# Performance work log

Measured on AMD Instinct MI355X. Metric: run time of the kernel, lower is better.

## Reference

```python
import jax, jax.numpy as jnp
import numpy as np

D = 1024

def setup_inputs() -> dict:
    key = jax.random.key(0)
    ks = jax.random.split(key, 9)
    B, S = 4, 2048
    s = 1.0 / np.sqrt(D)
    return {
        "query": jax.random.normal(ks[0], (B, S, D), jnp.float32),
        "key": jax.random.normal(ks[1], (B, S, D), jnp.float32),
        "value": jax.random.normal(ks[2], (B, S, D), jnp.float32),
        "Wq": jax.random.normal(ks[3], (D, D), jnp.float32) * s,
        "bq": jax.random.normal(ks[4], (D,), jnp.float32) * 0.01,
        "Wk": jax.random.normal(ks[5], (D, D), jnp.float32) * s,
        "bk": jax.random.normal(ks[6], (D,), jnp.float32) * 0.01,
        "Wv": jax.random.normal(ks[7], (D, D), jnp.float32) * s,
        "bv": jax.random.normal(ks[8], (D,), jnp.float32) * 0.01,
    }

def reference(query, key, value, Wq, bq, Wk, bk, Wv, bv):
    scale = 1.0 / (query.shape[-1] ** 0.5)
    q = jnp.einsum('bsd,ed->bse', query, Wq) + bq  # nn.Linear: x @ W.T + b
    k = jnp.einsum('bsd,ed->bse', key, Wk) + bk
    v = jnp.einsum('bsd,ed->bse', value, Wv) + bv
    scores = jnp.einsum('bqd,bkd->bqk', q, k) * scale  # [B, Sq, Skv]
    w = jax.nn.softmax(scores, axis=-1)
    return jnp.einsum('bqk,bkd->bqd', w, v)
```

## Files before the change

### kernel.cpp

```cpp
#include <hip/hip_runtime.h>

typedef __bf16 bf16x8 __attribute__((ext_vector_type(8)));
typedef float f32x4 __attribute__((ext_vector_type(4)));
typedef unsigned short u16x8 __attribute__((ext_vector_type(8)));

__device__ inline unsigned short f2bf(float f) {
  union { float f; unsigned u; } a; a.f = f;
  return (unsigned short)((a.u + 0x7fffu + ((a.u >> 16) & 1u)) >> 16);
}
__device__ inline float bf2f(unsigned short h) {
  union { unsigned u; float f; } a; a.u = ((unsigned)h) << 16;
  return a.f;
}

__global__ __launch_bounds__(256) void cvtW(const float* __restrict__ Wq,
                                            const float* __restrict__ Wk,
                                            const float* __restrict__ Wv,
                                            unsigned short* __restrict__ Wb) {
  int i = blockIdx.x * 256 + threadIdx.x;
  int idx = i >> 18;
  int off = i & 262143;
  const float* s = (idx == 0) ? Wq : ((idx == 1) ? Wk : Wv);
  float4 v = ((const float4*)s)[off];
  ushort4 o;
  o.x = f2bf(v.x); o.y = f2bf(v.y); o.z = f2bf(v.z); o.w = f2bf(v.w);
  ((ushort4*)(Wb + idx * 1048576))[off] = o;
}

#define G2L(gp, lp) __builtin_amdgcn_global_load_lds( \
    (const __attribute__((address_space(1))) void*)(gp), \
    (__attribute__((address_space(3))) void*)(lp), 16, 0, 0)

#define MFMA_(d, a, b) d = __builtin_amdgcn_mfma_f32_16x16x32_bf16(a, b, d, 0, 0, 0)
#define SB0() __builtin_amdgcn_sched_barrier(0)
#define LGKM(n) do { asm volatile("s_waitcnt lgkmcnt(" #n ")" ::: "memory"); SB0(); } while (0)
#define VMC(n) do { asm volatile("s_waitcnt vmcnt(" #n ")" ::: "memory"); SB0(); } while (0)

struct PJ {
  const float* A0; const float* A1; const float* A2;
  const unsigned short* B;
  unsigned short* outQ; unsigned short* outK; unsigned short* outV;
  const float* biasQ; const float* biasK; const float* biasV;
};

__global__ __launch_bounds__(256) void gemmP(PJ p) {
  extern __shared__ char smem[];
  char* smA = smem;
  char* smB = smem + 32768;
  const int tid = threadIdx.x, lane = tid & 63, wid = tid >> 6;
  const int wm = wid >> 1, wn = wid & 1;

  int orig = blockIdx.x + 8 * (blockIdx.y + 64 * blockIdx.z);
  int wg = (orig & 7) * 192 + (orig >> 3);
  int bx = wg & 7; int t2 = wg >> 3; int by = t2 & 63; int z = t2 >> 6;
  const int m0 = by << 7, n0 = bx << 7;

  const float* Az = (z == 0) ? p.A0 : ((z == 1) ? p.A1 : p.A2);

  const char* srcA0 = (const char*)Az + ((long long)m0 + (tid >> 4)) * 4096
                    + ((tid & 15) << 4);
  const int trow = tid >> 3;
  const int cs = (((tid & 7) ^ (trow & 7)) << 4);
  const char* srcB = (const char*)(p.B + (long long)z * 1048576
                                   + (long long)(n0 + trow) * 1024) + cs;

  const int aRowB = (((wm << 6) + (lane & 15)) << 7);
  const int bRowB = (((wn << 6) + (lane & 15)) << 7);
  const int csw = (lane & 7) << 4;
  const int ck0 = (((lane >> 4) << 4)) ^ csw;
  const int ck1 = ((((lane >> 4) << 4)) | 64) ^ csw;

  f32x4 acc[4][4];
#pragma unroll
  for (int i = 0; i < 4; ++i)
#pragma unroll
    for (int j = 0; j < 4; ++j) acc[i][j] = (f32x4){0.f, 0.f, 0.f, 0.f};

  float4 aregA[8], aregB[8];
  bf16x8 aLo[2][2], aHi[2][2], bLo[2][2], bHi[2][2];

  auto ldA = [&](int t, float4 (&ar)[8]) {
    const char* s = srcA0 + (long long)t * 256;
#pragma unroll
    for (int c = 0; c < 8; ++c)
      ar[c] = *(const float4*)(s + (long long)c * 65536);
  };
  auto wrA = [&](int t, float4 (&ar)[8]) {
    char* dA = smA + ((t & 1) << 14);
    const int g = (tid & 15) >> 1;
    const int hb = (tid & 1) << 3;
#pragma unroll
    for (int c = 0; c < 8; ++c) {
      const int rc = (c << 4) + (tid >> 4);
      float4 v = ar[c];
      union { __bf16 b[4]; ushort4 u; } o;
      o.b[0] = (__bf16)v.x; o.b[1] = (__bf16)v.y;
      o.b[2] = (__bf16)v.z; o.b[3] = (__bf16)v.w;
      *(ushort4*)(dA + (rc << 7) + ((g ^ (rc & 7)) << 4) + hb) = o.u;
    }
  };
  auto stageB = [&](int t, int b) {
    char* dB = smB + (b << 14) + (tid << 4);
    const char* sB = srcB + (long long)t * 128;
#pragma unroll
    for (int c = 0; c < 4; ++c)
      G2L(sB + (long long)c * 65536, dB + (c << 12));
  };
  auto readAh = [&](int b, int half, bf16x8 (&dst)[2][2]) {
    const char* ra = smA + (b << 14) + aRowB + (half << 12);
#pragma unroll
    for (int mi = 0; mi < 2; ++mi) {
      dst[mi][0] = *(const bf16x8*)(ra + (mi << 11) + ck0);
      dst[mi][1] = *(const bf16x8*)(ra + (mi << 11) + ck1);
    }
  };
  auto readBh = [&](int b, int half, bf16x8 (&dst)[2][2]) {
    const char* rb = smB + (b << 14) + bRowB + (half << 12);
#pragma unroll
    for (int ni = 0; ni < 2; ++ni) {
      dst[ni][0] = *(const bf16x8*)(rb + (ni << 11) + ck0);
      dst[ni][1] = *(const bf16x8*)(rb + (ni << 11) + ck1);
    }
  };
  auto quad = [&](int qa, int qb, bf16x8 (&A)[2][2], bf16x8 (&B)[2][2]) {
    __builtin_amdgcn_s_setprio(1);
#pragma unroll
    for (int mi = 0; mi < 2; ++mi)
#pragma unroll
      for (int ni = 0; ni < 2; ++ni) {
        MFMA_(acc[qa * 2 + mi][qb * 2 + ni], A[mi][0], B[ni][0]);
        MFMA_(acc[qa * 2 + mi][qb * 2 + ni], A[mi][1], B[ni][1]);
      }
    __builtin_amdgcn_s_setprio(0);
  };

  const int NT = 16;
  int b0 = 0, b1 = 1, b2 = 2;

  ldA(0, aregA); stageB(0, 0);
  ldA(1, aregB); stageB(1, 1);
  VMC(12);
  wrA(0, aregA);
  LGKM(0);
  __builtin_amdgcn_s_barrier();
  readAh(0, 0, aLo); readBh(0, 0, bLo);
  SB0();

  auto body = [&](int t, float4 (&arW)[8], float4 (&arL)[8]) {
    const bool pf1 = (t + 1) < NT, pf2 = (t + 2) < NT;
    if (pf2) { ldA(t + 2, arL); stageB(t + 2, b2); }
    readAh(t & 1, 1, aHi);
    SB0();
    LGKM(4);
    quad(0, 0, aLo, bLo);
    readBh(b0, 1, bHi);
    SB0();
    LGKM(4);
    quad(1, 0, aHi, bLo);
    LGKM(0);
    quad(0, 1, aLo, bHi);
    quad(1, 1, aHi, bHi);
    if (pf2) { VMC(12); }
    else     { VMC(0);  }
    if (pf1) wrA(t + 1, arW);
    LGKM(0);
    __builtin_amdgcn_s_barrier();
    if (pf1) { readAh((t + 1) & 1, 0, aLo); readBh(b1, 0, bLo); }
    SB0();
    int tmp = b0; b0 = b1; b1 = b2; b2 = tmp;
  };
  for (int t = 0; t < NT; t += 2) { body(t, aregB, aregA); body(t + 1, aregA, aregB); }

  const int c0 = lane & 15, r0 = (lane >> 4) << 2;
  if (z < 2) {
    unsigned short* O = (z == 0) ? p.outQ : p.outK;
    const float* bias = (z == 0) ? p.biasQ : p.biasK;
#pragma unroll
    for (int mi = 0; mi < 4; ++mi) {
      const int grow = m0 + (wm << 6) + (mi << 4) + r0;
#pragma unroll
      for (int ni = 0; ni < 4; ++ni) {
        const int gcol = n0 + (wn << 6) + (ni << 4) + c0;
        const float bb = bias[gcol];
#pragma unroll
        for (int rr = 0; rr < 4; ++rr)
          O[(long long)(grow + rr) * 1024 + gcol] = f2bf(acc[mi][ni][rr] + bb);
      }
    }
  } else {
#pragma unroll
    for (int mi = 0; mi < 4; ++mi) {
      const int grow = m0 + (wm << 6) + (mi << 4) + r0;
      const int bb = grow >> 11, s = grow & 2047;
#pragma unroll
      for (int ni = 0; ni < 4; ++ni) {
        const int d = n0 + (wn << 6) + (ni << 4) + c0;
        const float ba = p.biasV[d];
        ushort4 pk;
        pk.x = f2bf(acc[mi][ni][0] + ba);
        pk.y = f2bf(acc[mi][ni][1] + ba);
        pk.z = f2bf(acc[mi][ni][2] + ba);
        pk.w = f2bf(acc[mi][ni][3] + ba);
        *(ushort4*)(p.outV + ((long long)bb << 21) + (long long)d * 2048 + s) = pk;
      }
    }
  }
}

#define EPI_SCALE 1
#define EPI_OUT 2

struct GP {
  const unsigned short* A;
  const unsigned short* B;
  unsigned short* C;
  long long batchA, batchB, batchC;
  int lda, ldb, ldc, K;
  float scale;
};

template<int BM, int BN, int WMW, int WNW, int EPI>
__global__ __launch_bounds__(512, 2) void gemm2(GP p) {
  constexpr int NWN = BN / WNW;
  constexpr int AMF = WMW / 16, BNF = WNW / 16;
  constexpr int AH = AMF / 2, BH = BNF / 2;
  constexpr int AF_N = AH * 2;
  constexpr int NBA = BM / 64, NBB = BN / 64;
  static_assert((BM / WMW) * NWN == 8, "8 waves");
  static_assert(BNF == 4, "lgkm immediates assume BNF==4");

  extern __shared__ char smem[];
  char* smA = smem;
  char* smB = smem + 2 * BM * 128;

  const int tid = threadIdx.x;
  const int lane = tid & 63;
  const int wid = tid >> 6;
  const int wm = wid / NWN, wn = wid % NWN;

  const int gx = gridDim.x, gy = gridDim.y;
  const int nwg = gx * gy * (int)gridDim.z;
  int orig = blockIdx.x + gx * (blockIdx.y + gy * blockIdx.z);
  int qq = nwg >> 3, rr_ = nwg & 7;
  int xcd = orig & 7, sl = orig >> 3;
  int wg = (xcd < rr_ ? xcd * (qq + 1) : rr_ * (qq + 1) + (xcd - rr_) * qq) + sl;
  int bx = wg % gx;
  int t2 = wg / gx;
  int by = t2 % gy;
  int z  = t2 / gy;

  const int m0 = by * BM, n0 = bx * BN;

  const long long lda2 = (long long)p.lda * 2;
  const long long ldb2 = (long long)p.ldb * 2;
  const char* Abase = (const char*)(p.A + (long long)z * p.batchA) + (long long)m0 * lda2;
  const char* Bbase = (const char*)(p.B + (long long)z * p.batchB) + (long long)n0 * ldb2;

  const int trow = tid >> 3;
  const int cs = (((tid & 7) ^ (trow & 7)) << 4);
  const char* srcA = Abase + (long long)trow * lda2 + cs;
  const char* srcB = Bbase + (long long)trow * ldb2 + cs;

  const int NT = p.K >> 6;

  const int aRowB = ((wm * WMW + (lane & 15)) << 7);
  const int bRowB = ((wn * WNW + (lane & 15)) << 7);
  const int csw = (lane & 7) << 4;
  const int ck0 = (((lane >> 4) << 4)) ^ csw;
  const int ck1 = ((((lane >> 4) << 4)) | 64) ^ csw;

  f32x4 acc[AMF][BNF];
#pragma unroll
  for (int i = 0; i < AMF; ++i)
#pragma unroll
    for (int j = 0; j < BNF; ++j) acc[i][j] = (f32x4){0.f, 0.f, 0.f, 0.f};

  bf16x8 aLo[AH][2], aHi[AH][2], bLo[BH][2], bHi[BH][2];

  auto stage = [&](int t) {
    char* dA = smA + (t & 1) * (BM * 128) + (tid << 4);
    char* dB = smB + (t & 1) * (BN * 128) + (tid << 4);
    const char* sA = srcA + (long long)t * 128;
    const char* sB = srcB + (long long)t * 128;
#pragma unroll
    for (int c = 0; c < NBA; ++c) G2L(sA + (long long)c * (lda2 << 6), dA + c * 8192);
#pragma unroll
    for (int c = 0; c < NBB; ++c) G2L(sB + (long long)c * (ldb2 << 6), dB + c * 8192);
  };
  auto readAh = [&](int t, int half, bf16x8 (&dst)[AH][2]) {
    const char* ra = smA + (t & 1) * (BM * 128) + aRowB + half * (AH * 2048);
#pragma unroll
    for (int mi = 0; mi < AH; ++mi) {
      dst[mi][0] = *(const bf16x8*)(ra + mi * 2048 + ck0);
      dst[mi][1] = *(const bf16x8*)(ra + mi * 2048 + ck1);
    }
  };
  auto readBh = [&](int t, int half, bf16x8 (&dst)[BH][2]) {
    const char* rb = smB + (t & 1) * (BN * 128) + bRowB + half * (BH * 2048);
#pragma unroll
    for (int ni = 0; ni < BH; ++ni) {
      dst[ni][0] = *(const bf16x8*)(rb + ni * 2048 + ck0);
      dst[ni][1] = *(const bf16x8*)(rb + ni * 2048 + ck1);
    }
  };
  auto quad = [&](int qa, int qb, bf16x8 (&A)[AH][2], bf16x8 (&B)[BH][2]) {
    __builtin_amdgcn_s_setprio(1);
#pragma unroll
    for (int mi = 0; mi < AH; ++mi)
#pragma unroll
      for (int ni = 0; ni < BH; ++ni) {
        MFMA_(acc[qa * AH + mi][qb * BH + ni], A[mi][0], B[ni][0]);
        MFMA_(acc[qa * AH + mi][qb * BH + ni], A[mi][1], B[ni][1]);
      }
    __builtin_amdgcn_s_setprio(0);
  };

  stage(0); stage(1);
  if constexpr (NBA + NBB == 8) VMC(8); else VMC(6);
  __builtin_amdgcn_s_barrier();
  readAh(0, 0, aLo); readBh(0, 0, bLo);
  SB0();

  for (int t = 0; t < NT; ++t) {
    readAh(t, 1, aHi);
    SB0();
    if constexpr (AF_N == 8) LGKM(8); else LGKM(4);
    quad(0, 0, aLo, bLo);
    readBh(t, 1, bHi);
    SB0();
    LGKM(4);
    quad(1, 0, aHi, bLo);
    LGKM(0);
    quad(0, 1, aLo, bHi);
    quad(1, 1, aHi, bHi);
    VMC(0);
    __builtin_amdgcn_s_barrier();
    if (t + 2 < NT) stage(t + 2);
    if (t + 1 < NT) { readAh(t + 1, 0, aLo); readBh(t + 1, 0, bLo); }
    SB0();
  }

  const int c0 = lane & 15;
  const int r0 = (lane >> 4) << 2;
  if constexpr (EPI == EPI_SCALE) {
    unsigned short* Cz = p.C + (long long)z * p.batchC;
#pragma unroll
    for (int mi = 0; mi < AMF; ++mi) {
      const int grow = m0 + wm * WMW + (mi << 4) + r0;
#pragma unroll
      for (int ni = 0; ni < BNF; ++ni) {
        const int gcol = n0 + wn * WNW + (ni << 4) + c0;
#pragma unroll
        for (int rr = 0; rr < 4; ++rr)
          Cz[(long long)(grow + rr) * p.ldc + gcol] = f2bf(acc[mi][ni][rr] * p.scale);
      }
    }
  } else {
    float* Cz = (float*)p.C + (long long)z * p.batchC;
#pragma unroll
    for (int mi = 0; mi < AMF; ++mi) {
      const int grow = m0 + wm * WMW + (mi << 4) + r0;
#pragma unroll
      for (int ni = 0; ni < BNF; ++ni) {
        const int gcol = n0 + wn * WNW + (ni << 4) + c0;
#pragma unroll
        for (int rr = 0; rr < 4; ++rr)
          Cz[(long long)(grow + rr) * p.ldc + gcol] = acc[mi][ni][rr] * p.scale;
      }
    }
  }
}

__global__ __launch_bounds__(512) void gemmPV(GP p) {
  constexpr int ABUF = 256 * 128, BBUF = 128 * 128;
  extern __shared__ char smem[];
  char* smA = smem;
  char* smB = smem + 3 * ABUF;

  const int tid = threadIdx.x;
  const int lane = tid & 63;
  const int wid = tid >> 6;
  const int wm = wid >> 1, wn = wid & 1;

  const int gx = gridDim.x, gy = gridDim.y;
  const int nwg = gx * gy * (int)gridDim.z;
  int orig = blockIdx.x + gx * (blockIdx.y + gy * blockIdx.z);
  int qq = nwg >> 3, rr_ = nwg & 7;
  int xcd = orig & 7, sl = orig >> 3;
  int wg = (xcd < rr_ ? xcd * (qq + 1) : rr_ * (qq + 1) + (xcd - rr_) * qq) + sl;
  int bx = wg % gx;
  int t2 = wg / gx;
  int by = t2 % gy;
  int z  = t2 / gy;

  const int m0 = by * 256, n0 = bx * 128;

  const long long lda2 = (long long)p.lda * 2;
  const long long ldb2 = (long long)p.ldb * 2;
  const char* Abase = (const char*)(p.A + (long long)z * p.batchA) + (long long)m0 * lda2;
  const char* Bbase = (const char*)(p.B + (long long)z * p.batchB) + (long long)n0 * ldb2;

  const int trow = tid >> 3;
  const int cs = (((tid & 7) ^ (trow & 7)) << 4);
  const char* srcA = Abase + (long long)trow * lda2 + cs;
  const char* srcB = Bbase + (long long)trow * ldb2 + cs;

  const int NT = p.K >> 6;

  const int aRowB = ((wm * 64 + (lane & 15)) << 7);
  const int bRowB = ((wn * 64 + (lane & 15)) << 7);
  const int csw = (lane & 7) << 4;
  const int ck0 = (((lane >> 4) << 4)) ^ csw;
  const int ck1 = ((((lane >> 4) << 4)) | 64) ^ csw;

  f32x4 acc[4][4];
#pragma unroll
  for (int i = 0; i < 4; ++i)
#pragma unroll
    for (int j = 0; j < 4; ++j) acc[i][j] = (f32x4){0.f, 0.f, 0.f, 0.f};

  bf16x8 aLo[2][2], aHi[2][2], bLo[2][2], bHi[2][2];

  auto stage = [&](int t, int b) {
    char* dA = smA + b * ABUF + (tid << 4);
    char* dB = smB + b * BBUF + (tid << 4);
    const char* sA = srcA + (long long)t * 128;
    const char* sB = srcB + (long long)t * 128;
#pragma unroll
    for (int c = 0; c < 4; ++c) G2L(sA + (long long)c * (lda2 << 6), dA + c * 8192);
#pragma unroll
    for (int c = 0; c < 2; ++c) G2L(sB + (long long)c * (ldb2 << 6), dB + c * 8192);
  };
  auto readAh = [&](int b, int half, bf16x8 (&dst)[2][2]) {
    const char* ra = smA + b * ABUF + aRowB + half * 4096;
#pragma unroll
    for (int mi = 0; mi < 2; ++mi) {
      dst[mi][0] = *(const bf16x8*)(ra + mi * 2048 + ck0);
      dst[mi][1] = *(const bf16x8*)(ra + mi * 2048 + ck1);
    }
  };
  auto readBh = [&](int b, int half, bf16x8 (&dst)[2][2]) {
    const char* rb = smB + b * BBUF + bRowB + half * 4096;
#pragma unroll
    for (int ni = 0; ni < 2; ++ni) {
      dst[ni][0] = *(const bf16x8*)(rb + ni * 2048 + ck0);
      dst[ni][1] = *(const bf16x8*)(rb + ni * 2048 + ck1);
    }
  };
  auto quad = [&](int qa, int qb, bf16x8 (&A)[2][2], bf16x8 (&B)[2][2]) {
    __builtin_amdgcn_s_setprio(1);
#pragma unroll
    for (int mi = 0; mi < 2; ++mi)
#pragma unroll
      for (int ni = 0; ni < 2; ++ni) {
        MFMA_(acc[qa * 2 + mi][qb * 2 + ni], A[mi][0], B[ni][0]);
        MFMA_(acc[qa * 2 + mi][qb * 2 + ni], A[mi][1], B[ni][1]);
      }
    __builtin_amdgcn_s_setprio(0);
  };

  int b0 = 0, b1 = 1, b2 = 2;

  stage(0, 0); stage(1, 1);
  VMC(6);
  __builtin_amdgcn_s_barrier();
  readAh(0, 0, aLo); readBh(0, 0, bLo);
  SB0();

  for (int t = 0; t < NT; ++t) {
    if (t + 2 < NT) stage(t + 2, b2);
    readAh(b0, 1, aHi);
    SB0();
    LGKM(4);
    quad(0, 0, aLo, bLo);
    readBh(b0, 1, bHi);
    SB0();
    LGKM(4);
    quad(1, 0, aHi, bLo);
    LGKM(0);
    quad(0, 1, aLo, bHi);
    quad(1, 1, aHi, bHi);
    if (t + 2 < NT) { VMC(6); }
    else            { VMC(0); }
    __builtin_amdgcn_s_barrier();
    if (t + 1 < NT) { readAh(b1, 0, aLo); readBh(b1, 0, bLo); }
    SB0();
    int tmp = b0; b0 = b1; b1 = b2; b2 = tmp;
  }

  const int c0 = lane & 15;
  const int r0 = (lane >> 4) << 2;
  float* Cz = (float*)p.C + (long long)z * p.batchC;
#pragma unroll
  for (int mi = 0; mi < 4; ++mi) {
    const int grow = m0 + wm * 64 + (mi << 4) + r0;
#pragma unroll
    for (int ni = 0; ni < 4; ++ni) {
      const int gcol = n0 + wn * 64 + (ni << 4) + c0;
#pragma unroll
      for (int rr = 0; rr < 4; ++rr)
        Cz[(long long)(grow + rr) * p.ldc + gcol] = acc[mi][ni][rr] * p.scale;
    }
  }
}

__global__ __launch_bounds__(256) void softmax_rows(unsigned short* __restrict__ S) {
  const size_t row = blockIdx.x;
  unsigned short* pp = S + row * 2048;
  const int t = threadIdx.x, lane = t & 63, wave = t >> 6;
  u16x8 h = ((const u16x8*)pp)[t];
  float x[8];
#pragma unroll
  for (int j = 0; j < 8; ++j) x[j] = bf2f(h[j]);
  float m = x[0];
#pragma unroll
  for (int j = 1; j < 8; ++j) m = fmaxf(m, x[j]);
#pragma unroll
  for (int off = 32; off >= 1; off >>= 1) m = fmaxf(m, __shfl_xor(m, off, 64));
  __shared__ float rmax[4], rsum[4];
  if (lane == 0) rmax[wave] = m;
  __syncthreads();
  m = fmaxf(fmaxf(rmax[0], rmax[1]), fmaxf(rmax[2], rmax[3]));
  float e[8], sum = 0.f;
#pragma unroll
  for (int j = 0; j < 8; ++j) { e[j] = __expf(x[j] - m); sum += e[j]; }
#pragma unroll
  for (int off = 32; off >= 1; off >>= 1) sum += __shfl_xor(sum, off, 64);
  if (lane == 0) rsum[wave] = sum;
  __syncthreads();
  sum = rsum[0] + rsum[1] + rsum[2] + rsum[3];
  const float inv = 1.f / sum;
  u16x8 o;
#pragma unroll
  for (int j = 0; j < 8; ++j) o[j] = f2bf(e[j] * inv);
  ((u16x8*)pp)[t] = o;
}

extern "C" void kernel_launch(void* const* d_in, const int* in_sizes, int n_in,
                              void* d_out, int out_size, void* d_ws, size_t ws_size,
                              hipStream_t stream) {
  const float* q  = (const float*)d_in[0];
  const float* k  = (const float*)d_in[1];
  const float* v  = (const float*)d_in[2];
  const float* Wq = (const float*)d_in[3];
  const float* bq = (const float*)d_in[4];
  const float* Wk = (const float*)d_in[5];
  const float* bk = (const float*)d_in[6];
  const float* Wv = (const float*)d_in[7];
  const float* bv = (const float*)d_in[8];

  unsigned short* S  = (unsigned short*)d_ws;
  unsigned short* Wb = S + 16777216;
  unsigned short* qb = Wb + 3145728;
  unsigned short* kb = qb + 8388608;
  unsigned short* vT = kb + 8388608;

  (void)hipFuncSetAttribute((const void*)gemmP,
      hipFuncAttributeMaxDynamicSharedMemorySize, 81920);
  (void)hipFuncSetAttribute((const void*)gemm2<256,256,128,64,EPI_SCALE>,
      hipFuncAttributeMaxDynamicSharedMemorySize, 131072);
  (void)hipFuncSetAttribute((const void*)gemmPV,
      hipFuncAttributeMaxDynamicSharedMemorySize, 147456);

  cvtW<<<3072, 256, 0, stream>>>(Wq, Wk, Wv, Wb);

  PJ pj{};
  pj.A0 = q; pj.A1 = k; pj.A2 = v;
  pj.B = Wb;
  pj.outQ = qb; pj.outK = kb; pj.outV = vT;
  pj.biasQ = bq; pj.biasK = bk; pj.biasV = bv;
  gemmP<<<dim3(8, 64, 3), 256, 81920, stream>>>(pj);

  GP gs{};
  gs.A = qb; gs.batchA = 2097152; gs.lda = 1024;
  gs.B = kb; gs.batchB = 2097152; gs.ldb = 1024;
  gs.C = S;  gs.batchC = 4194304; gs.ldc = 2048;
  gs.K = 1024; gs.scale = 0.03125f;
  gemm2<256,256,128,64,EPI_SCALE><<<dim3(8, 8, 4), 512, 131072, stream>>>(gs);

  softmax_rows<<<8192, 256, 0, stream>>>(S);

  GP gv{};
  gv.A = S;  gv.batchA = 4194304; gv.lda = 2048;
  gv.B = vT; gv.batchB = 2097152; gv.ldb = 2048;
  gv.C = (unsigned short*)d_out; gv.batchC = 2097152; gv.ldc = 1024;
  gv.K = 2048; gv.scale = 1.f;
  gemmPV<<<dim3(8, 8, 4), 512, 147456, stream>>>(gv);
}
```

Baseline: 167.3 us.

## Halve projection GEMM K-tile to 32 with paired-row swizzled LDS layout

The QKV projection GEMM now uses a K step of 32 instead of 64 per iteration (32 iterations instead of 16). Two 64-byte rows are packed into each 128-byte LDS row with a new XOR swizzle, and the A/B staging and fragment reads are rewritten to match. Dynamic shared memory drops from 80KB to 40KB and per-thread prefetch registers are halved, which should allow more resident workgroups per CU. The cost is twice as many barriers and loop iterations, plus less work per synchronization.

```diff
diff --git a/kernel.cpp b/kernel.cpp
--- a/kernel.cpp
+++ b/kernel.cpp
@@ -46,7 +46,7 @@
 __global__ __launch_bounds__(256) void gemmP(PJ p) {
   extern __shared__ char smem[];
   char* smA = smem;
-  char* smB = smem + 32768;
+  char* smB = smem + 16384;
   const int tid = threadIdx.x, lane = tid & 63, wid = tid >> 6;
   const int wm = wid >> 1, wn = wid & 1;
 
@@ -57,18 +57,20 @@
 
   const float* Az = (z == 0) ? p.A0 : ((z == 1) ? p.A1 : p.A2);
 
-  const char* srcA0 = (const char*)Az + ((long long)m0 + (tid >> 4)) * 4096
-                    + ((tid & 15) << 4);
-  const int trow = tid >> 3;
-  const int cs = (((tid & 7) ^ (trow & 7)) << 4);
+  const char* srcA0 = (const char*)Az + ((long long)m0 + (tid >> 3)) * 4096
+                    + ((tid & 7) << 4);
+  const int L0 = tid >> 3;
+  const int sgB = (tid & 7) ^ (L0 & 7);
   const char* srcB = (const char*)(p.B + (long long)z * 1048576
-                                   + (long long)(n0 + trow) * 1024) + cs;
-
-  const int aRowB = (((wm << 6) + (lane & 15)) << 7);
-  const int bRowB = (((wn << 6) + (lane & 15)) << 7);
-  const int csw = (lane & 7) << 4;
-  const int ck0 = (((lane >> 4) << 4)) ^ csw;
-  const int ck1 = ((((lane >> 4) << 4)) | 64) ^ csw;
+                     + (long long)(n0 + 2 * L0 + (sgB >> 2)) * 1024)
+                   + ((sgB & 3) << 4);
+
+  const int kqW = (tid & 7) >> 1;
+  const int hW = (tid & 1) << 3;
+
+  const int kh = lane >> 4;
+  const int Ra0 = (wm << 6) + (lane & 15);
+  const int Rb0 = (wn << 6) + (lane & 15);
 
   f32x4 acc[4][4];
 #pragma unroll
@@ -76,96 +78,96 @@
 #pragma unroll
     for (int j = 0; j < 4; ++j) acc[i][j] = (f32x4){0.f, 0.f, 0.f, 0.f};
 
-  float4 aregA[8], aregB[8];
-  bf16x8 aLo[2][2], aHi[2][2], bLo[2][2], bHi[2][2];
-
-  auto ldA = [&](int t, float4 (&ar)[8]) {
-    const char* s = srcA0 + (long long)t * 256;
-#pragma unroll
-    for (int c = 0; c < 8; ++c)
-      ar[c] = *(const float4*)(s + (long long)c * 65536);
-  };
-  auto wrA = [&](int t, float4 (&ar)[8]) {
-    char* dA = smA + ((t & 1) << 14);
-    const int g = (tid & 15) >> 1;
-    const int hb = (tid & 1) << 3;
-#pragma unroll
-    for (int c = 0; c < 8; ++c) {
-      const int rc = (c << 4) + (tid >> 4);
+  float4 aregA[4], aregB[4];
+  bf16x8 aLo[2], aHi[2], bLo[2], bHi[2];
+
+  auto ldA = [&](int t, float4 (&ar)[4]) {
+    const char* s = srcA0 + (long long)t * 128;
+#pragma unroll
+    for (int c = 0; c < 4; ++c)
+      ar[c] = *(const float4*)(s + (long long)c * 131072);
+  };
+  auto wrA = [&](int t, float4 (&ar)[4]) {
+    char* dA = smA + ((t & 1) << 13);
+#pragma unroll
+    for (int c = 0; c < 4; ++c) {
+      const int r = (c << 5) + (tid >> 3);
+      const int L = r >> 1, par = r & 1;
       float4 v = ar[c];
-      union { __bf16 b[4]; ushort4 u; } o;
+      union { __bf16 b[4]; unsigned long long u; } o;
       o.b[0] = (__bf16)v.x; o.b[1] = (__bf16)v.y;
       o.b[2] = (__bf16)v.z; o.b[3] = (__bf16)v.w;
-      *(ushort4*)(dA + (rc << 7) + ((g ^ (rc & 7)) << 4) + hb) = o.u;
+      *(unsigned long long*)(dA + (L << 7)
+          + ((((par << 2) | kqW) ^ (L & 7)) << 4) + hW) = o.u;
     }
   };
   auto stageB = [&](int t, int b) {
-    char* dB = smB + (b << 14) + (tid << 4);
-    const char* sB = srcB + (long long)t * 128;
-#pragma unroll
-    for (int c = 0; c < 4; ++c)
-      G2L(sB + (long long)c * 65536, dB + (c << 12));
-  };
-  auto readAh = [&](int b, int half, bf16x8 (&dst)[2][2]) {
-    const char* ra = smA + (b << 14) + aRowB + (half << 12);
-#pragma unroll
-    for (int mi = 0; mi < 2; ++mi) {
-      dst[mi][0] = *(const bf16x8*)(ra + (mi << 11) + ck0);
-      dst[mi][1] = *(const bf16x8*)(ra + (mi << 11) + ck1);
-    }
-  };
-  auto readBh = [&](int b, int half, bf16x8 (&dst)[2][2]) {
-    const char* rb = smB + (b << 14) + bRowB + (half << 12);
-#pragma unroll
-    for (int ni = 0; ni < 2; ++ni) {
-      dst[ni][0] = *(const bf16x8*)(rb + (ni << 11) + ck0);
-      dst[ni][1] = *(const bf16x8*)(rb + (ni << 11) + ck1);
-    }
-  };
-  auto quad = [&](int qa, int qb, bf16x8 (&A)[2][2], bf16x8 (&B)[2][2]) {
+    char* dB = smB + (b << 13) + (tid << 4);
+    const char* sB = srcB + (long long)t * 64;
+#pragma unroll
+    for (int c = 0; c < 2; ++c)
+      G2L(sB + (long long)c * 64 * 2048, dB + (c << 12));
+  };
+  auto readA = [&](int b, int half, bf16x8 (&dst)[2]) {
+    const char* ra = smA + (b << 13);
+#pragma unroll
+    for (int f = 0; f < 2; ++f) {
+      const int R = Ra0 + ((half * 2 + f) << 4);
+      dst[f] = *(const bf16x8*)(ra + ((R >> 1) << 7)
+               + (((((R & 1) << 2) | kh) ^ ((R >> 1) & 7)) << 4));
+    }
+  };
+  auto readB = [&](int b, int half, bf16x8 (&dst)[2]) {
+    const char* rb = smB + (b << 13);
+#pragma unroll
+    for (int f = 0; f < 2; ++f) {
+      const int R = Rb0 + ((half * 2 + f) << 4);
+      dst[f] = *(const bf16x8*)(rb + ((R >> 1) << 7)
+               + (((((R & 1) << 2) | kh) ^ ((R >> 1) & 7)) << 4));
+    }
+  };
+  auto quad = [&](int qa, int qb, bf16x8 (&A)[2], bf16x8 (&B)[2]) {
     __builtin_amdgcn_s_setprio(1);
 #pragma unroll
     for (int mi = 0; mi < 2; ++mi)
 #pragma unroll
-      for (int ni = 0; ni < 2; ++ni) {
-        MFMA_(acc[qa * 2 + mi][qb * 2 + ni], A[mi][0], B[ni][0]);
-        MFMA_(acc[qa * 2 + mi][qb * 2 + ni], A[mi][1], B[ni][1]);
-      }
+      for (int ni = 0; ni < 2; ++ni)
+        MFMA_(acc[qa * 2 + mi][qb * 2 + ni], A[mi], B[ni]);
     __builtin_amdgcn_s_setprio(0);
   };
 
-  const int NT = 16;
+  const int NT = 32;
   int b0 = 0, b1 = 1, b2 = 2;
 
   ldA(0, aregA); stageB(0, 0);
   ldA(1, aregB); stageB(1, 1);
-  VMC(12);
+  VMC(6);
   wrA(0, aregA);
   LGKM(0);
   __builtin_amdgcn_s_barrier();
-  readAh(0, 0, aLo); readBh(0, 0, bLo);
+  readA(0, 0, aLo); readB(0, 0, bLo);
   SB0();
 
-  auto body = [&](int t, float4 (&arW)[8], float4 (&arL)[8]) {
+  auto body = [&](int t, float4 (&arW)[4], float4 (&arL)[4]) {
     const bool pf1 = (t + 1) < NT, pf2 = (t + 2) < NT;
     if (pf2) { ldA(t + 2, arL); stageB(t + 2, b2); }
-    readAh(t & 1, 1, aHi);
-    SB0();
-    LGKM(4);
+    readA(t & 1, 1, aHi);
+    SB0();
+    LGKM(2);
     quad(0, 0, aLo, bLo);
-    readBh(b0, 1, bHi);
-    SB0();
-    LGKM(4);
+    readB(b0, 1, bHi);
+    SB0();
+    LGKM(2);
     quad(1, 0, aHi, bLo);
     LGKM(0);
     quad(0, 1, aLo, bHi);
     quad(1, 1, aHi, bHi);
-    if (pf2) { VMC(12); }
-    else     { VMC(0);  }
+    if (pf2) { VMC(6); }
+    else     { VMC(0); }
     if (pf1) wrA(t + 1, arW);
     LGKM(0);
     __builtin_amdgcn_s_barrier();
-    if (pf1) { readAh((t + 1) & 1, 0, aLo); readBh(b1, 0, bLo); }
+    if (pf1) { readA((t + 1) & 1, 0, aLo); readB(b1, 0, bLo); }
     SB0();
     int tmp = b0; b0 = b1; b1 = b2; b2 = tmp;
   };
@@ -556,7 +558,7 @@
   unsigned short* vT = kb + 8388608;
 
   (void)hipFuncSetAttribute((const void*)gemmP,
-      hipFuncAttributeMaxDynamicSharedMemorySize, 81920);
+      hipFuncAttributeMaxDynamicSharedMemorySize, 40960);
   (void)hipFuncSetAttribute((const void*)gemm2<256,256,128,64,EPI_SCALE>,
       hipFuncAttributeMaxDynamicSharedMemorySize, 131072);
   (void)hipFuncSetAttribute((const void*)gemmPV,
@@ -569,7 +571,7 @@
   pj.B = Wb;
   pj.outQ = qb; pj.outK = kb; pj.outV = vT;
   pj.biasQ = bq; pj.biasK = bk; pj.biasV = bv;
-  gemmP<<<dim3(8, 64, 3), 256, 81920, stream>>>(pj);
+  gemmP<<<dim3(8, 64, 3), 256, 40960, stream>>>(pj);
 
   GP gs{};
   gs.A = qb; gs.batchA = 2097152; gs.lda = 1024;
```

Result: slower. 174.2 us (+4.1%).
